# Kernel optimization log

Measured on AMD Instinct MI355X. Metric: run time of the kernel, lower is better.

Reference implementation:

```python
import jax, jax.numpy as jnp
import numpy as np
from jax import lax

SLOPE = 25.0  # snntorch surrogate.fast_sigmoid default slope
NUM_STEPS = 25

@jax.custom_vjp
def spike_fn(x):
    # forward: heaviside(x > 0); backward: fast-sigmoid surrogate grad
    return (x > 0).astype(x.dtype)

def _spike_fwd(x):
    return spike_fn(x), x

def _spike_bwd(x, g):
    return (g / (SLOPE * jnp.abs(x) + 1.0) ** 2,)

spike_fn.defvjp(_spike_fwd, _spike_bwd)


def setup_inputs() -> dict:
    key = jax.random.key(0)
    ks = jax.random.split(key, 6)
    B, NI, NH, NO = 32768, 256, 1024, 1
    x = jax.random.normal(ks[0], (B, NI), dtype=jnp.float32)
    W1 = jax.random.normal(ks[1], (NH, NI), dtype=jnp.float32) / np.sqrt(NI)
    b1 = jax.random.normal(ks[2], (NH,), dtype=jnp.float32) * 0.01
    W2 = jax.random.normal(ks[3], (NO, NH), dtype=jnp.float32) / np.sqrt(NH)
    b2 = jax.random.normal(ks[4], (NO,), dtype=jnp.float32) * 0.01
    beta = jnp.asarray(0.9, dtype=jnp.float32)       # learn_beta=True scalar
    thr = jnp.full((NH,), 1.0, dtype=jnp.float32)    # learn_threshold=True
    return {"x": x, "W1": W1, "b1": b1, "W2": W2, "b2": b2, "beta": beta, "thr": thr}


def reference(x, W1, b1, W2, b2, beta, thr):
    x1 = x @ W1.T + b1                      # [B, NH], constant input each step
    beta_c = jnp.clip(beta, 0.0, 1.0)

    def step(carry, _):
        mem, spk_sum = carry
        reset = spike_fn(mem - thr)         # reset based on previous membrane
        mem_new = beta_c * mem + x1 - reset * thr  # subtract reset mechanism
        spk = spike_fn(mem_new - thr)
        return (mem_new, spk_sum + spk), None

    init = (jnp.zeros_like(x1), jnp.zeros_like(x1))
    (mem, spk_sum), _ = lax.scan(step, init, None, length=NUM_STEPS)
    return spk_sum @ W2.T + b2              # [B, 1]
```

## Files before the change

### kernel.cpp

```cpp
#include <hip/hip_runtime.h>


#define NI 256
#define NH 1024
#define NSTEPS 25
#define BT 128
#define BK 32
#define NTILES (NI / BK)
#define BPR 36
#define RW 40

typedef _Float16 half8 __attribute__((ext_vector_type(8)));
typedef _Float16 half4 __attribute__((ext_vector_type(4)));
typedef float float4v __attribute__((ext_vector_type(4)));

__device__ __forceinline__ unsigned f2k(float f) {
    unsigned u = __float_as_uint(f);
    return (u >> 31) ? ~u : (u | 0x80000000u);
}
__device__ __forceinline__ float k2f(unsigned k) {
    unsigned u = (k & 0x80000000u) ? (k & 0x7FFFFFFFu) : ~k;
    return __uint_as_float(u);
}

__device__ __forceinline__ int lif_count(float x1, float beta, float th) {
    float mem = 0.f;
    float spk = (0.f > th) ? 1.f : 0.f;
    int c = 0;
#pragma unroll
    for (int t = 0; t < NSTEPS; t++) {
        mem = fmaf(spk, -th, fmaf(beta, mem, x1));
        spk = (mem > th) ? 1.f : 0.f;
        c += (mem > th);
    }
    return c;
}

__device__ __forceinline__ void split8(const float* src, half8* hi, half8* lo) {
    float4v a = *(const float4v*)src;
    float4v b = *(const float4v*)(src + 4);
#pragma unroll
    for (int e = 0; e < 4; e++) {
        _Float16 h = (_Float16)a[e];
        (*hi)[e] = h;
        (*lo)[e] = (_Float16)(a[e] - (float)h);
        h = (_Float16)b[e];
        (*hi)[e + 4] = h;
        (*lo)[e + 4] = (_Float16)(b[e] - (float)h);
    }
}


__global__ __launch_bounds__(256) void snn_prep(
    const float* __restrict__ x, const float* __restrict__ W1,
    const float* __restrict__ thr, const float* __restrict__ betap,
    const float* __restrict__ b1, const float* __restrict__ b2,
    float* __restrict__ out, float* __restrict__ bp,
    _Float16* __restrict__ whp, _Float16* __restrict__ wlp,
    _Float16* __restrict__ xhp, _Float16* __restrict__ xlp, int B)
{
    const int tid = threadIdx.x;
    const int XB = B / 8;
    int bid = blockIdx.x;

    if (bid < XB) {
        const int G = bid * 256 + tid;
        const int band = G >> 12;
        const int rem = G & 4095;
        const int kt = rem >> 9;
        const int rem2 = rem & 511;
        const int r8 = rem2 >> 6, quad = (rem2 >> 4) & 3, col = rem2 & 15;
        const float* src = x + (size_t)(band * 128 + r8 * 16 + col) * NI + kt * 32 + quad * 8;
        half8 hi, lo;
        split8(src, &hi, &lo);
        ((half8*)xhp)[G] = hi;
        ((half8*)xlp)[G] = lo;
        return;
    }
    bid -= XB;
    if (bid < 128) {
        const int G = bid * 256 + tid;
        const int band = G >> 12;
        const int rem = G & 4095;
        const int kt = rem >> 9;
        const int rem2 = rem & 511;
        const int r8 = rem2 >> 6, quad = (rem2 >> 4) & 3, col = rem2 & 15;
        const float* src = W1 + (size_t)(band * 128 + r8 * 16 + col) * NI + kt * 32 + quad * 8;
        half8 hi, lo;
        split8(src, &hi, &lo);
        ((half8*)whp)[G] = hi;
        ((half8*)wlp)[G] = lo;
        return;
    }
    bid -= 128;
    if (bid < 100) {
        const int idx = bid * 256 + tid;
        const int h = idx / NSTEPS;
        const int k = idx % NSTEPS + 1;
        const float th = thr[h];
        const float bj = b1[h];
        float beta = betap[0];
        beta = beta < 0.f ? 0.f : (beta > 1.f ? 1.f : beta);
        unsigned lo = f2k(-3.0e38f), hi = f2k(3.0e38f);
        float res;
        if (lif_count(k2f(hi) + bj, beta, th) < k) {
            res = 3.0e38f;
        } else if (lif_count(k2f(lo) + bj, beta, th) >= k) {
            res = -3.0e38f;
        } else {
#pragma unroll 1
            for (int it = 0; it < 32; it++) {
                unsigned mid = lo + ((hi - lo) >> 1);
                if (lif_count(k2f(mid) + bj, beta, th) >= k) hi = mid; else lo = mid;
            }
            res = k2f(hi);
        }
        bp[h * 32 + (k - 1)] = res;
        return;
    }
    bid -= 100;
    {
        const int i = bid * 256 + tid;
        if (i < B) out[i] = b2[0];
    }
}

__global__ __launch_bounds__(256, 2) void snn_main_fast(
    const _Float16* __restrict__ xhp, const _Float16* __restrict__ xlp,
    const _Float16* __restrict__ whp, const _Float16* __restrict__ wlp,
    const float* __restrict__ W2, const float* __restrict__ bp,
    float* __restrict__ out)
{
    __shared__ float smem[128 * BPR];

    const int tid  = threadIdx.x;
    const int w    = tid >> 6;
    const int lane = tid & 63;
    const int col  = lane & 15;
    const int quad = lane >> 4;
    const int wbb  = (w >> 1) * 64;
    const int whh  = (w & 1) * 64;
    const int bband = blockIdx.x;
    const int hband = blockIdx.y;
    const int b0 = bband * BT;
    const int h0 = hband * BT;
    const int loff = quad * 16 + col;

    const half8* xh = (const half8*)xhp + (size_t)bband * 4096 + (w >> 1) * 256 + loff;
    const half8* xl = (const half8*)xlp + (size_t)bband * 4096 + (w >> 1) * 256 + loff;
    const half8* wh = (const half8*)whp + (size_t)hband * 4096 + (w & 1) * 256 + loff;
    const half8* wl = (const half8*)wlp + (size_t)hband * 4096 + (w & 1) * 256 + loff;

    float* bpl = smem;
    {
        const int hl = tid >> 1, q = (tid & 1) * 4;
#pragma unroll
        for (int rep = 0; rep < 4; rep++) {
            float4v v = *(const float4v*)&bp[(h0 + hl) * 32 + q + 8 * rep];
            *(float4v*)&bpl[hl * BPR + q + 8 * rep] = v;
        }
    }

    float4v acc[4][4];
#pragma unroll
    for (int i = 0; i < 4; i++)
#pragma unroll
        for (int j = 0; j < 4; j++) acc[i][j] = (float4v){0.f, 0.f, 0.f, 0.f};

#pragma unroll 2
    for (int kt = 0; kt < NTILES; kt++) {
        const int gi = kt * 512;
        half8 ah[4], al[4], bh[4], bl[4];
#pragma unroll
        for (int i = 0; i < 4; i++) {
            ah[i] = xh[gi + i * 64];
            al[i] = xl[gi + i * 64];
        }
#pragma unroll
        for (int j = 0; j < 4; j++) {
            bh[j] = wh[gi + j * 64];
            bl[j] = wl[gi + j * 64];
        }
#pragma unroll
        for (int j = 0; j < 4; j++)
#pragma unroll
            for (int i = 0; i < 4; i++) {
                acc[i][j] = __builtin_amdgcn_mfma_f32_16x16x32_f16(ah[i], bh[j], acc[i][j], 0, 0, 0);
                acc[i][j] = __builtin_amdgcn_mfma_f32_16x16x32_f16(ah[i], bl[j], acc[i][j], 0, 0, 0);
                acc[i][j] = __builtin_amdgcn_mfma_f32_16x16x32_f16(al[i], bh[j], acc[i][j], 0, 0, 0);
            }
    }

    __syncthreads();

    float part[16];
#pragma unroll
    for (int e = 0; e < 16; e++) part[e] = 0.f;

#pragma unroll
    for (int j = 0; j < 4; j++) {
        const int hl = whh + 16 * j + col;
        const float w2 = W2[h0 + hl];
        float4v c[7];
#pragma unroll
        for (int q = 0; q < 7; q++)
            c[q] = *(const float4v*)&bpl[hl * BPR + 4 * q];
        float x1[16];
        int cnt[16];
#pragma unroll
        for (int e = 0; e < 16; e++) {
            x1[e] = acc[e >> 2][j][e & 3];
            cnt[e] = 0;
        }
#pragma unroll
        for (int k = 0; k < NSTEPS; k++) {
            const float ck = c[k >> 2][k & 3];
#pragma unroll
            for (int e = 0; e < 16; e++) cnt[e] += (x1[e] >= ck) ? 1 : 0;
        }
#pragma unroll
        for (int e = 0; e < 16; e++)
            part[e] = fmaf((float)cnt[e], w2, part[e]);
    }

    __syncthreads();
    float* red = smem;
#pragma unroll
    for (int e = 0; e < 16; e++) {
        const int row = wbb + 16 * (e >> 2) + 4 * quad + (e & 3);
        red[row * 33 + (w & 1) * 16 + col] = part[e];
    }
    __syncthreads();
    if (tid < BT) {
        float s = 0.f;
#pragma unroll
        for (int c2 = 0; c2 < 32; c2++) s += red[tid * 33 + c2];
        atomicAdd(&out[b0 + tid], s);
    }
}


__global__ __launch_bounds__(256) void snn_prep_small(
    const float* __restrict__ thr, const float* __restrict__ betap,
    const float* __restrict__ b2, float* __restrict__ out,
    float* __restrict__ bp, int B)
{
    const int tid = threadIdx.x;
    int bid = blockIdx.x;
    if (bid < 100) {
        const int idx = bid * 256 + tid;
        const int h = idx / NSTEPS;
        const int k = idx % NSTEPS + 1;
        const float th = thr[h];
        float beta = betap[0];
        beta = beta < 0.f ? 0.f : (beta > 1.f ? 1.f : beta);
        unsigned lo = f2k(-3.0e38f), hi = f2k(3.0e38f);
        float res;
        if (lif_count(k2f(hi), beta, th) < k) res = 3.0e38f;
        else if (lif_count(k2f(lo), beta, th) >= k) res = -3.0e38f;
        else {
#pragma unroll 1
            for (int it = 0; it < 32; it++) {
                unsigned mid = lo + ((hi - lo) >> 1);
                if (lif_count(k2f(mid), beta, th) >= k) hi = mid; else lo = mid;
            }
            res = k2f(hi);
        }
        bp[(k - 1) * NH + h] = res;
        return;
    }
    bid -= 100;
    const int i = bid * 256 + tid;
    if (i < B) out[i] = b2[0];
}

__global__ __launch_bounds__(256, 3) void snn_main_fb(
    const float* __restrict__ x, const float* __restrict__ W1,
    const float* __restrict__ b1, const float* __restrict__ W2,
    const float* __restrict__ bp, float* __restrict__ out)
{
    __shared__ __align__(16) _Float16 lds[4 * BT * RW];
    _Float16* xh = lds;
    _Float16* xl = lds + BT * RW;
    _Float16* wh = lds + 2 * BT * RW;
    _Float16* wl = lds + 3 * BT * RW;

    const int tid  = threadIdx.x;
    const int w    = tid >> 6;
    const int lane = tid & 63;
    const int col  = lane & 15;
    const int quad = lane >> 4;
    const int wbb  = (w >> 1) * 64;
    const int whh  = (w & 1) * 64;
    const int b0 = blockIdx.x * BT;
    const int h0 = blockIdx.y * BT;

    float4v acc[4][4];
#pragma unroll
    for (int i = 0; i < 4; i++)
#pragma unroll
        for (int j = 0; j < 4; j++) acc[i][j] = (float4v){0.f, 0.f, 0.f, 0.f};

    const int r0 = tid >> 3;
    const int c4 = tid & 7;
    const float* xrow = x + (size_t)(b0 + r0) * NI + 4 * c4;
    const float* wrow = W1 + (size_t)(h0 + r0) * NI + 4 * c4;

    for (int kt = 0; kt < NTILES; kt++) {
        const int ko = kt * BK;
        float4v vx[4], vw[4];
#pragma unroll
        for (int p = 0; p < 4; p++) {
            vx[p] = *(const float4v*)(xrow + (size_t)(32 * p) * NI + ko);
            vw[p] = *(const float4v*)(wrow + (size_t)(32 * p) * NI + ko);
        }
        __syncthreads();
#pragma unroll
        for (int p = 0; p < 4; p++) {
            const int row = r0 + 32 * p;
            half4 hx, lx, hw, lw;
#pragma unroll
            for (int q = 0; q < 4; q++) {
                float v = vx[p][q];
                _Float16 h = (_Float16)v;
                hx[q] = h;
                lx[q] = (_Float16)(v - (float)h);
                v = vw[p][q];
                h = (_Float16)v;
                hw[q] = h;
                lw[q] = (_Float16)(v - (float)h);
            }
            *(half4*)&xh[row * RW + 4 * c4] = hx;
            *(half4*)&xl[row * RW + 4 * c4] = lx;
            *(half4*)&wh[row * RW + 4 * c4] = hw;
            *(half4*)&wl[row * RW + 4 * c4] = lw;
        }
        __syncthreads();

        half8 ah[4], al[4];
#pragma unroll
        for (int i = 0; i < 4; i++) {
            ah[i] = *(const half8*)&xh[(wbb + 16 * i + col) * RW + 8 * quad];
            al[i] = *(const half8*)&xl[(wbb + 16 * i + col) * RW + 8 * quad];
        }
#pragma unroll
        for (int j = 0; j < 4; j++) {
            half8 bh = *(const half8*)&wh[(whh + 16 * j + col) * RW + 8 * quad];
            half8 bl = *(const half8*)&wl[(whh + 16 * j + col) * RW + 8 * quad];
#pragma unroll
            for (int i = 0; i < 4; i++) {
                acc[i][j] = __builtin_amdgcn_mfma_f32_16x16x32_f16(ah[i], bh, acc[i][j], 0, 0, 0);
                acc[i][j] = __builtin_amdgcn_mfma_f32_16x16x32_f16(ah[i], bl, acc[i][j], 0, 0, 0);
                acc[i][j] = __builtin_amdgcn_mfma_f32_16x16x32_f16(al[i], bh, acc[i][j], 0, 0, 0);
            }
        }
    }

    __syncthreads();
    float* bpl = (float*)lds;
    for (int n = tid; n < NSTEPS * 128; n += 256)
        bpl[n] = bp[(n >> 7) * NH + h0 + (n & 127)];
    __syncthreads();

    float part[16];
#pragma unroll
    for (int e = 0; e < 16; e++) part[e] = 0.f;
#pragma unroll
    for (int j = 0; j < 4; j++) {
        const int hl = whh + 16 * j + col;
        const int h = h0 + hl;
        const float w2 = W2[h];
        const float bj = b1[h];
        float x1[16];
        int cnt[16];
#pragma unroll
        for (int e = 0; e < 16; e++) {
            x1[e] = acc[e >> 2][j][e & 3] + bj;
            cnt[e] = 0;
        }
#pragma unroll
        for (int k = 0; k < NSTEPS; k++) {
            const float c = bpl[k * 128 + hl];
#pragma unroll
            for (int e = 0; e < 16; e++) cnt[e] += (x1[e] >= c) ? 1 : 0;
        }
#pragma unroll
        for (int e = 0; e < 16; e++)
            part[e] = fmaf((float)cnt[e], w2, part[e]);
    }

    __syncthreads();
    float* red = (float*)lds;
#pragma unroll
    for (int e = 0; e < 16; e++) {
        const int row = wbb + 16 * (e >> 2) + 4 * quad + (e & 3);
        red[row * 33 + (w & 1) * 16 + col] = part[e];
    }
    __syncthreads();
    if (tid < BT) {
        float s = 0.f;
#pragma unroll
        for (int c = 0; c < 32; c++) s += red[tid * 33 + c];
        atomicAdd(&out[b0 + tid], s);
    }
}

extern "C" void kernel_launch(void* const* d_in, const int* in_sizes, int n_in,
                              void* d_out, int out_size, void* d_ws, size_t ws_size,
                              hipStream_t stream) {
    const float* x    = (const float*)d_in[0];
    const float* W1   = (const float*)d_in[1];
    const float* b1   = (const float*)d_in[2];
    const float* W2   = (const float*)d_in[3];
    const float* b2   = (const float*)d_in[4];
    const float* beta = (const float*)d_in[5];
    const float* thr  = (const float*)d_in[6];
    float* out = (float*)d_out;

    const int B = in_sizes[0] / NI;

    char* ws = (char*)d_ws;
    float*     bp  = (float*)ws;
    size_t off = (size_t)NH * 32 * 4;
    _Float16* whp = (_Float16*)(ws + off);  off += (size_t)NH * NI * 2;
    _Float16* wlp = (_Float16*)(ws + off);  off += (size_t)NH * NI * 2;
    _Float16* xhp = (_Float16*)(ws + off);  off += (size_t)B * NI * 2;
    _Float16* xlp = (_Float16*)(ws + off);  off += (size_t)B * NI * 2;
    const size_t ws_need = off;

    if (ws_size >= ws_need) {
        const int nblk = B / 8 + 128 + 100 + (B + 255) / 256;
        snn_prep<<<nblk, 256, 0, stream>>>(x, W1, thr, beta, b1, b2, out,
                                           bp, whp, wlp, xhp, xlp, B);
        dim3 grid(B / BT, NH / BT);
        snn_main_fast<<<grid, 256, 0, stream>>>(xhp, xlp, whp, wlp, W2, bp, out);
    } else {
        snn_prep_small<<<100 + (B + 255) / 256, 256, 0, stream>>>(thr, beta, b2, out, bp, B);
        dim3 grid(B / BT, NH / BT);
        snn_main_fb<<<grid, 256, 0, stream>>>(x, W1, b1, W2, bp, out);
    }
}
```

Measured before the change: 175.8 us.

## Replace linear threshold scan with branchless binary search over sorted breakpoints

The per-element spike count is now found with a 5-step branchless binary search into the sorted per-neuron breakpoint table in shared memory, replacing the 25-compare linear scan. The table is padded to 32 entries with a large sentinel and uses a stride of 33 to reduce bank conflicts on the data-dependent LDS reads. Launch bounds are raised to 3 blocks per SIMD to increase occupancy. The cost is gathered LDS loads per element in place of register-resident comparisons, plus tighter register pressure.

```diff
diff --git a/kernel.cpp b/kernel.cpp
--- a/kernel.cpp
+++ b/kernel.cpp
@@ -7,7 +7,7 @@
 #define BT 128
 #define BK 32
 #define NTILES (NI / BK)
-#define BPR 36
+#define BPS 33
 #define RW 40
 
 typedef _Float16 half8 __attribute__((ext_vector_type(8)));
@@ -125,13 +125,13 @@
     }
 }
 
-__global__ __launch_bounds__(256, 2) void snn_main_fast(
+__global__ __launch_bounds__(256, 3) void snn_main_fast(
     const _Float16* __restrict__ xhp, const _Float16* __restrict__ xlp,
     const _Float16* __restrict__ whp, const _Float16* __restrict__ wlp,
     const float* __restrict__ W2, const float* __restrict__ bp,
     float* __restrict__ out)
 {
-    __shared__ float smem[128 * BPR];
+    __shared__ float smem[128 * BPS];
 
     const int tid  = threadIdx.x;
     const int w    = tid >> 6;
@@ -152,13 +152,12 @@
     const half8* wl = (const half8*)wlp + (size_t)hband * 4096 + (w & 1) * 256 + loff;
 
     float* bpl = smem;
-    {
-        const int hl = tid >> 1, q = (tid & 1) * 4;
-#pragma unroll
-        for (int rep = 0; rep < 4; rep++) {
-            float4v v = *(const float4v*)&bp[(h0 + hl) * 32 + q + 8 * rep];
-            *(float4v*)&bpl[hl * BPR + q + 8 * rep] = v;
-        }
+#pragma unroll
+    for (int rep = 0; rep < 16; rep++) {
+        const int n = tid + 256 * rep;
+        const int hl = n >> 5, k = n & 31;
+        const float v = bp[(h0 + hl) * 32 + k];
+        bpl[hl * BPS + k] = (k < NSTEPS) ? v : 3.0e38f;
     }
 
     float4v acc[4][4];
@@ -201,26 +200,25 @@
     for (int j = 0; j < 4; j++) {
         const int hl = whh + 16 * j + col;
         const float w2 = W2[h0 + hl];
-        float4v c[7];
-#pragma unroll
-        for (int q = 0; q < 7; q++)
-            c[q] = *(const float4v*)&bpl[hl * BPR + 4 * q];
+        const float* pj = bpl + hl * BPS;
         float x1[16];
-        int cnt[16];
+        int mo[16];
 #pragma unroll
         for (int e = 0; e < 16; e++) {
             x1[e] = acc[e >> 2][j][e & 3];
-            cnt[e] = 0;
-        }
-#pragma unroll
-        for (int k = 0; k < NSTEPS; k++) {
-            const float ck = c[k >> 2][k & 3];
-#pragma unroll
-            for (int e = 0; e < 16; e++) cnt[e] += (x1[e] >= ck) ? 1 : 0;
+            mo[e] = 0;
+        }
+#pragma unroll
+        for (int bstep = 16; bstep >= 1; bstep >>= 1) {
+#pragma unroll
+            for (int e = 0; e < 16; e++) {
+                const float c = pj[mo[e] + bstep - 1];
+                mo[e] += (x1[e] >= c) ? bstep : 0;
+            }
         }
 #pragma unroll
         for (int e = 0; e < 16; e++)
-            part[e] = fmaf((float)cnt[e], w2, part[e]);
+            part[e] = fmaf((float)mo[e], w2, part[e]);
     }
 
     __syncthreads();
```

Result: faster. 157.0 us (-10.7%).
